# Kernel optimization log

Measured on AMD Instinct MI355X. Metric: run time of the kernel, lower is better.

The kernel has to match this reference:

```python
import jax, jax.numpy as jnp
import numpy as np

N_NODES = 100000      # total nodes across batch (50 graphs x 2000 nodes)
N_EDGES = 1600000     # avg degree 16
D = 64                # input_dim = hidden dims = output_dim
L = 3                 # number of GIN layers actually executed
NUM_GRAPHS = 50
NODES_PER_GRAPH = 2000
CAT_D = L * D         # 192, concat of hidden layer outputs


def setup_inputs() -> dict:
    key = jax.random.key(0)
    ks = jax.random.split(key, 12)
    s = 1.0 / np.sqrt(D)          # torch Linear init scale
    s2 = 1.0 / np.sqrt(CAT_D)
    return {
        "x": jax.random.normal(ks[0], (N_NODES, D), jnp.float32),
        "edge_index": jax.random.randint(ks[1], (2, N_EDGES), 0, N_NODES),
        "edge_weight": jax.random.uniform(ks[2], (N_EDGES,), jnp.float32),
        "batch": jnp.repeat(jnp.arange(NUM_GRAPHS), NODES_PER_GRAPH),  # sorted graph ids
        "W1": jax.random.uniform(ks[3], (L, D, D), jnp.float32, -s, s),
        "b1": jax.random.uniform(ks[4], (L, D), jnp.float32, -s, s),
        "W2": jax.random.uniform(ks[5], (L, D, D), jnp.float32, -s, s),
        "b2": jax.random.uniform(ks[6], (L, D), jnp.float32, -s, s),
        "eps": jnp.zeros((L,), jnp.float32),  # train_eps init 0.0
        "lin_w": jax.random.uniform(ks[7], (CAT_D, D), jnp.float32, -s2, s2),
        "lin_b": jax.random.uniform(ks[8], (D,), jnp.float32, -s2, s2),
    }


def reference(x, edge_index, edge_weight, batch, W1, b1, W2, b2, eps, lin_w, lin_b):
    src, dst = edge_index[0], edge_index[1]
    ew = edge_weight[:, None]
    h = x
    hiddens = []
    for l in range(L):
        # weighted GIN: aggregate sum_j w_ij * h_j at destination nodes
        agg = jax.ops.segment_sum(h[src] * ew, dst, num_segments=N_NODES)
        z = (1.0 + eps[l]) * h + agg
        # GIN MLP: Linear -> LeakyReLU -> Linear
        z = jax.nn.leaky_relu(z @ W1[l] + b1[l]) @ W2[l] + b2[l]
        hiddens.append(z)              # hiddens store pre-activation conv output
        h = jax.nn.leaky_relu(z)       # activation feeds next layer (dropout=0)
    h_cat = jnp.concatenate(hiddens, axis=-1)          # [N, 192]
    pooled = jax.ops.segment_sum(h_cat, batch, num_segments=NUM_GRAPHS)  # global_add_pool
    return pooled @ lin_w + lin_b                      # [NUM_GRAPHS, D]
```

## Files before the change

### kernel.cpp

```cpp
#include <hip/hip_runtime.h>

#define N_NODES 100000
#define N_EDGES 1600000
#define DD 64
#define NLAYER 3
#define NUM_GRAPHS 50
#define NODES_PER_GRAPH 2000
#define CAT_D (NLAYER * DD)
#define MROWS 80
#define MLP_THREADS 320
#define LPITCH 72

#define NPB 256
#define NB ((N_NODES + NPB - 1) / NPB)
#define BPAD 6144
#define ECHUNK 4096

#define GNODES 32
#define WECAP 288

typedef __attribute__((ext_vector_type(8))) short short8;
typedef __attribute__((ext_vector_type(4))) float float4v;

__device__ __forceinline__ unsigned short f2bf(float f) {
    unsigned u = __float_as_uint(f);
    unsigned r = u + 0x7FFF + ((u >> 16) & 1);
    return (unsigned short)(r >> 16);
}
__device__ __forceinline__ float bflo(unsigned u) {
    return __uint_as_float(u << 16);
}
__device__ __forceinline__ float bfhi(unsigned u) {
    return __uint_as_float(u & 0xFFFF0000u);
}

__global__ __launch_bounds__(256) void convert_x_kernel(
    const float* __restrict__ x, unsigned short* __restrict__ hx)
{
    int i = (blockIdx.x * blockDim.x + threadIdx.x) * 4;
    if (i + 3 < N_NODES * DD) {
        float4 v = *(const float4*)&x[i];
        hx[i]     = f2bf(v.x);
        hx[i + 1] = f2bf(v.y);
        hx[i + 2] = f2bf(v.z);
        hx[i + 3] = f2bf(v.w);
    }
}

__global__ __launch_bounds__(256) void convert_w_kernel(
    const float* __restrict__ W1, const float* __restrict__ W2,
    unsigned short* __restrict__ W1t, unsigned short* __restrict__ W2t,
    int* __restrict__ cursor)
{
    int idx = blockIdx.x * blockDim.x + threadIdx.x;
    if (idx < NB) cursor[idx] = idx * BPAD;
    if (idx >= 2 * NLAYER * DD * DD) return;
    int which = idx / (NLAYER * DD * DD);
    int rem = idx % (NLAYER * DD * DD);
    int l = rem / (DD * DD);
    int t = rem % (DD * DD);
    int n = t >> 6, k = t & 63;
    const float* W = which ? W2 : W1;
    unsigned short* Wt = which ? W2t : W1t;
    Wt[l * DD * DD + n * DD + k] = f2bf(W[l * DD * DD + k * DD + n]);
}

__global__ __launch_bounds__(256) void bin_kernel(
    const int* __restrict__ src, const int* __restrict__ dst,
    const float* __restrict__ ew, int* __restrict__ cursor,
    uint2* __restrict__ binned)
{
    __shared__ uint2 stage[ECHUNK];
    __shared__ unsigned short bkt[ECHUNK];
    __shared__ int cnt[512];
    __shared__ int base[512];
    __shared__ int ssum[256];
    __shared__ int gbase[512];

    const int tid = threadIdx.x;
    const int start = blockIdx.x * ECHUNK;
    const int count = min(ECHUNK, N_EDGES - start);

    cnt[tid] = 0;
    cnt[tid + 256] = 0;
    __syncthreads();

    unsigned pk1[16], pk2[16];
    int eb[16], er[16];
    #pragma unroll
    for (int k = 0; k < 16; ++k) {
        int i = tid + k * 256;
        if (i < count) {
            int e = start + i;
            int s = src[e];
            int d = dst[e];
            float w = ew[e];
            int b = d >> 8;
            pk1[k] = (unsigned)s | ((unsigned)(d & 255) << 17);
            pk2[k] = __float_as_uint(w);
            eb[k] = b;
            er[k] = atomicAdd(&cnt[b], 1);
        } else {
            eb[k] = -1;
        }
    }
    __syncthreads();

    int c0 = cnt[2 * tid], c1 = cnt[2 * tid + 1];
    ssum[tid] = c0 + c1;
    __syncthreads();
    for (int off = 1; off < 256; off <<= 1) {
        int x = (tid >= off) ? ssum[tid - off] : 0;
        __syncthreads();
        ssum[tid] += x;
        __syncthreads();
    }
    int ex = (tid > 0) ? ssum[tid - 1] : 0;
    base[2 * tid] = ex;
    base[2 * tid + 1] = ex + c0;

    if (2 * tid < NB && c0 > 0)     gbase[2 * tid]     = atomicAdd(&cursor[2 * tid], c0);
    if (2 * tid + 1 < NB && c1 > 0) gbase[2 * tid + 1] = atomicAdd(&cursor[2 * tid + 1], c1);
    __syncthreads();

    #pragma unroll
    for (int k = 0; k < 16; ++k) {
        if (eb[k] >= 0) {
            int p = base[eb[k]] + er[k];
            stage[p].x = pk1[k];
            stage[p].y = pk2[k];
            bkt[p] = (unsigned short)eb[k];
        }
    }
    __syncthreads();

    for (int i = tid; i < count; i += 256) {
        int b = bkt[i];
        binned[gbase[b] + (i - base[b])] = stage[i];
    }
}

__global__ __launch_bounds__(256) void localsort_kernel(
    const int* __restrict__ cursor, const uint2* __restrict__ binned,
    uint2* __restrict__ s_edge, int* __restrict__ beg, int* __restrict__ end)
{
    __shared__ int deg[NPB];
    __shared__ int rb[NPB];
    __shared__ int cur[NPB];

    const int nb = blockIdx.x;
    const int tid = threadIdx.x;
    const int bstart = nb * BPAD;
    const int count = cursor[nb] - bstart;

    deg[tid] = 0;
    __syncthreads();
    for (int i = tid; i < count; i += 256) {
        unsigned w = binned[bstart + i].x;
        atomicAdd(&deg[(w >> 17) & 255], 1);
    }
    __syncthreads();

    int v = deg[tid];
    rb[tid] = v;
    __syncthreads();
    for (int off = 1; off < 256; off <<= 1) {
        int x = (tid >= off) ? rb[tid - off] : 0;
        __syncthreads();
        rb[tid] += x;
        __syncthreads();
    }
    int ex = rb[tid] - v;
    cur[tid] = ex;
    int node = nb * NPB + tid;
    if (node < N_NODES) {
        beg[node] = bstart + ex;
        end[node] = bstart + ex + v;
    }
    __syncthreads();

    for (int i = tid; i < count; i += 256) {
        uint2 e = binned[bstart + i];
        int d = (e.x >> 17) & 255;
        int r = atomicAdd(&cur[d], 1);
        uint2 o;
        o.x = e.x & 0x1FFFF;
        o.y = e.y;
        s_edge[bstart + r] = o;
    }
}

__global__ __launch_bounds__(256) void gather_kernel(
    const uint4* __restrict__ h4, const int* __restrict__ beg,
    const int* __restrict__ end, const uint2* __restrict__ s_edge,
    const float* __restrict__ eps, int l, uint4* __restrict__ z4)
{
    __shared__ uint2 eds[4 * WECAP];

    const int w    = threadIdx.x >> 6;
    const int lane = threadIdx.x & 63;
    const int o    = lane >> 3;
    const int fl   = lane & 7;
    const int nbase = blockIdx.x * GNODES + w * 8;
    const int node  = nbase + o;

    const int ebeg = beg[nbase];
    const int cnt  = end[nbase + 7] - ebeg;
    uint2* wl = &eds[w * WECAP];
    const bool lds_ok = (cnt <= WECAP);
    if (lds_ok) {
        for (int i = lane; i < cnt; i += 64) wl[i] = s_edge[ebeg + i];
    }

    const int gbeg = beg[node];
    const int deg  = end[node] - gbeg;

    float acc[4][8];
    #pragma unroll
    for (int c = 0; c < 4; ++c)
        #pragma unroll
        for (int j = 0; j < 8; ++j) acc[c][j] = 0.f;

    const uint4* hfl = h4 + fl;

    if (lds_ok) {
        const int bi = gbeg - ebeg;
        for (int it = 0; it < deg; it += 4) {
            #pragma unroll
            for (int c = 0; c < 4; ++c) {
                bool ok = (it + c) < deg;
                int idx = ok ? (bi + it + c) : bi;
                uint2 p = wl[idx];
                float wv = ok ? __uint_as_float(p.y) : 0.f;
                uint4 r = hfl[(long)p.x * 8];
                acc[c][0] += bflo(r.x) * wv;  acc[c][1] += bfhi(r.x) * wv;
                acc[c][2] += bflo(r.y) * wv;  acc[c][3] += bfhi(r.y) * wv;
                acc[c][4] += bflo(r.z) * wv;  acc[c][5] += bfhi(r.z) * wv;
                acc[c][6] += bflo(r.w) * wv;  acc[c][7] += bfhi(r.w) * wv;
            }
        }
    } else {
        for (int it = 0; it < deg; it += 4) {
            #pragma unroll
            for (int c = 0; c < 4; ++c) {
                bool ok = (it + c) < deg;
                int idx = ok ? (gbeg + it + c) : gbeg;
                uint2 p = s_edge[idx];
                float wv = ok ? __uint_as_float(p.y) : 0.f;
                uint4 r = hfl[(long)p.x * 8];
                acc[c][0] += bflo(r.x) * wv;  acc[c][1] += bfhi(r.x) * wv;
                acc[c][2] += bflo(r.y) * wv;  acc[c][3] += bfhi(r.y) * wv;
                acc[c][4] += bflo(r.z) * wv;  acc[c][5] += bfhi(r.z) * wv;
                acc[c][6] += bflo(r.w) * wv;  acc[c][7] += bfhi(r.w) * wv;
            }
        }
    }

    float s[8];
    #pragma unroll
    for (int j = 0; j < 8; ++j)
        s[j] = (acc[0][j] + acc[1][j]) + (acc[2][j] + acc[3][j]);

    const float e1 = 1.0f + eps[l];
    uint4 selfr = hfl[(long)node * 8];
    float z0 = e1 * bflo(selfr.x) + s[0];
    float z1 = e1 * bfhi(selfr.x) + s[1];
    float z2 = e1 * bflo(selfr.y) + s[2];
    float z3 = e1 * bfhi(selfr.y) + s[3];
    float z4v = e1 * bflo(selfr.z) + s[4];
    float z5 = e1 * bfhi(selfr.z) + s[5];
    float z6 = e1 * bflo(selfr.w) + s[6];
    float z7 = e1 * bfhi(selfr.w) + s[7];
    uint4 ov;
    ov.x = (unsigned)f2bf(z0) | ((unsigned)f2bf(z1) << 16);
    ov.y = (unsigned)f2bf(z2) | ((unsigned)f2bf(z3) << 16);
    ov.z = (unsigned)f2bf(z4v) | ((unsigned)f2bf(z5) << 16);
    ov.w = (unsigned)f2bf(z6) | ((unsigned)f2bf(z7) << 16);
    z4[(long)node * 8 + fl] = ov;
}

__global__ __launch_bounds__(MLP_THREADS) void mlp_kernel(
    const unsigned short* __restrict__ z_in,
    const unsigned short* __restrict__ W1t, const unsigned short* __restrict__ W2t,
    const float* __restrict__ b1l, const float* __restrict__ b2l,
    int l, unsigned short* __restrict__ h_out, float* __restrict__ pooled)
{
    __shared__ __align__(16) unsigned short zs[MROWS * LPITCH];
    __shared__ __align__(16) unsigned short w1s[DD * LPITCH];
    __shared__ __align__(16) unsigned short w2s[DD * LPITCH];
    __shared__ float red[5 * DD];

    const int tid  = threadIdx.x;
    const int lane = tid & 63;
    const int w    = tid >> 6;
    const int m15  = lane & 15;
    const int quad = lane >> 4;
    const long base = (long)blockIdx.x * MROWS;

    for (int idx = tid; idx < MROWS * 8; idx += MLP_THREADS) {
        int row = idx >> 3, seg = idx & 7;
        *(int4*)&zs[row * LPITCH + seg * 8] =
            *(const int4*)&z_in[(base + row) * DD + seg * 8];
    }
    for (int idx = tid; idx < DD * 8; idx += MLP_THREADS) {
        int row = idx >> 3, seg = idx & 7;
        *(int4*)&w1s[row * LPITCH + seg * 8] =
            *(const int4*)&W1t[(size_t)l * DD * DD + row * DD + seg * 8];
        *(int4*)&w2s[row * LPITCH + seg * 8] =
            *(const int4*)&W2t[(size_t)l * DD * DD + row * DD + seg * 8];
    }
    __syncthreads();

    {
        short8 a0 = *(const short8*)&zs[(w * 16 + m15) * LPITCH + quad * 8];
        short8 a1 = *(const short8*)&zs[(w * 16 + m15) * LPITCH + 32 + quad * 8];
        #pragma unroll
        for (int n = 0; n < 4; ++n) {
            short8 b0 = *(const short8*)&w1s[(n * 16 + m15) * LPITCH + quad * 8];
            short8 b1 = *(const short8*)&w1s[(n * 16 + m15) * LPITCH + 32 + quad * 8];
            float4v acc = {0.f, 0.f, 0.f, 0.f};
            acc = __builtin_amdgcn_mfma_f32_16x16x32_bf16(a0, b0, acc, 0, 0, 0);
            acc = __builtin_amdgcn_mfma_f32_16x16x32_bf16(a1, b1, acc, 0, 0, 0);
            int col = n * 16 + m15;
            float bv = b1l[col];
            #pragma unroll
            for (int r = 0; r < 4; ++r) {
                int row = w * 16 + quad * 4 + r;
                float t = acc[r] + bv;
                t = t > 0.0f ? t : 0.01f * t;
                zs[row * LPITCH + col] = f2bf(t);
            }
        }
    }

    float psum[4];
    {
        short8 a0 = *(const short8*)&zs[(w * 16 + m15) * LPITCH + quad * 8];
        short8 a1 = *(const short8*)&zs[(w * 16 + m15) * LPITCH + 32 + quad * 8];
        #pragma unroll
        for (int n = 0; n < 4; ++n) {
            short8 b0 = *(const short8*)&w2s[(n * 16 + m15) * LPITCH + quad * 8];
            short8 b1 = *(const short8*)&w2s[(n * 16 + m15) * LPITCH + 32 + quad * 8];
            float4v acc = {0.f, 0.f, 0.f, 0.f};
            acc = __builtin_amdgcn_mfma_f32_16x16x32_bf16(a0, b0, acc, 0, 0, 0);
            acc = __builtin_amdgcn_mfma_f32_16x16x32_bf16(a1, b1, acc, 0, 0, 0);
            int col = n * 16 + m15;
            float bv = b2l[col];
            float ps = 0.0f;
            #pragma unroll
            for (int r = 0; r < 4; ++r) {
                int row = w * 16 + quad * 4 + r;
                float z2 = acc[r] + bv;
                ps += z2;
                float hv = z2 > 0.0f ? z2 : 0.01f * z2;
                zs[row * LPITCH + col] = f2bf(hv);
            }
            psum[n] = ps;
        }
    }
    #pragma unroll
    for (int n = 0; n < 4; ++n) {
        float v = psum[n];
        v += __shfl_xor(v, 16);
        v += __shfl_xor(v, 32);
        if (quad == 0) red[w * DD + n * 16 + m15] = v;
    }
    __syncthreads();

    if (h_out) {
        for (int idx = tid; idx < MROWS * 8; idx += MLP_THREADS) {
            int row = idx >> 3, seg = idx & 7;
            *(int4*)&h_out[(base + row) * DD + seg * 8] =
                *(const int4*)&zs[row * LPITCH + seg * 8];
        }
    }
    if (tid < DD) {
        float tot = red[tid] + red[DD + tid] + red[2 * DD + tid]
                  + red[3 * DD + tid] + red[4 * DD + tid];
        int g = blockIdx.x / (NODES_PER_GRAPH / MROWS);
        atomicAdd(&pooled[g * CAT_D + l * DD + tid], tot);
    }
}

__global__ __launch_bounds__(64) void final_kernel(
    const float* __restrict__ pooled, const float* __restrict__ lin_w,
    const float* __restrict__ lin_b, float* __restrict__ out)
{
    int g = blockIdx.x;
    int j = threadIdx.x;
    float acc = lin_b[j];
    for (int k = 0; k < CAT_D; ++k)
        acc += pooled[g * CAT_D + k] * lin_w[k * DD + j];
    out[g * DD + j] = acc;
}

extern "C" void kernel_launch(void* const* d_in, const int* in_sizes, int n_in,
                              void* d_out, int out_size, void* d_ws, size_t ws_size,
                              hipStream_t stream)
{
    const float* x     = (const float*)d_in[0];
    const int*   ei    = (const int*)d_in[1];
    const float* ew    = (const float*)d_in[2];
    const float* W1    = (const float*)d_in[4];
    const float* b1    = (const float*)d_in[5];
    const float* W2    = (const float*)d_in[6];
    const float* b2    = (const float*)d_in[7];
    const float* eps   = (const float*)d_in[8];
    const float* lin_w = (const float*)d_in[9];
    const float* lin_b = (const float*)d_in[10];
    float* out = (float*)d_out;

    const int* src = ei;
    const int* dst = ei + N_EDGES;

    char* wsb = (char*)d_ws;
    size_t off = 0;
    auto alloc = [&](size_t bytes) -> void* {
        off = (off + 15) & ~(size_t)15;
        void* p = wsb + off;
        off += bytes;
        return p;
    };
    unsigned short* hX   = (unsigned short*)alloc((size_t)N_NODES * DD * 2);
    unsigned short* hA   = (unsigned short*)alloc((size_t)N_NODES * DD * 2);
    unsigned short* zbuf = (unsigned short*)alloc((size_t)N_NODES * DD * 2);
    unsigned short* W1t  = (unsigned short*)alloc((size_t)NLAYER * DD * DD * 2);
    unsigned short* W2t  = (unsigned short*)alloc((size_t)NLAYER * DD * DD * 2);
    float* pooled        = (float*)alloc((size_t)NUM_GRAPHS * CAT_D * 4);
    int*   cursor        = (int*)alloc((size_t)NB * 4);
    int*   beg           = (int*)alloc((size_t)N_NODES * 4);
    int*   end_          = (int*)alloc((size_t)N_NODES * 4);
    uint2* binned        = (uint2*)alloc((size_t)NB * BPAD * 8);
    uint2* s_edge        = (uint2*)alloc((size_t)NB * BPAD * 8);

    convert_x_kernel<<<(N_NODES * DD / 4 + 255) / 256, 256, 0, stream>>>(x, hX);
    convert_w_kernel<<<(2 * NLAYER * DD * DD + 255) / 256, 256, 0, stream>>>(
        W1, W2, W1t, W2t, cursor);

    bin_kernel<<<(N_EDGES + ECHUNK - 1) / ECHUNK, 256, 0, stream>>>(
        src, dst, ew, cursor, binned);
    localsort_kernel<<<NB, 256, 0, stream>>>(cursor, binned, s_edge, beg, end_);

    hipMemsetAsync(pooled, 0, NUM_GRAPHS * CAT_D * sizeof(float), stream);

    const unsigned short* h_ins[3]  = { hX, hA, hX };
    unsigned short*       h_outs[3] = { hA, hX, nullptr };
    for (int l = 0; l < NLAYER; ++l) {
        gather_kernel<<<N_NODES / GNODES, 256, 0, stream>>>(
            (const uint4*)h_ins[l], beg, end_, s_edge, eps, l,
            (uint4*)zbuf);

        mlp_kernel<<<N_NODES / MROWS, MLP_THREADS, 0, stream>>>(
            zbuf, W1t, W2t,
            b1 + (size_t)l * DD, b2 + (size_t)l * DD,
            l, h_outs[l], pooled);
    }

    final_kernel<<<NUM_GRAPHS, 64, 0, stream>>>(pooled, lin_w, lin_b, out);
}
```

Measured before the change: 277.3 us.

## Store node features in fp8 and pack edge index with bf16 weight

Node feature buffers are now stored as fp8 (e4m3 via the cvt_pk_fp8 builtins) instead of bf16, which halves the bytes fetched per neighbour in the gather. The sorted edge records shrink from 8 to 4 bytes by packing a 17-bit source index with a 15-bit truncated bf16 weight. The per-warp LDS edge cache capacity is enlarged to match. These changes target the memory-bound gather, but fp8 features and a sign-dropped, truncated weight lose considerable precision and may break the accuracy tolerance.

```diff
diff --git a/kernel.cpp b/kernel.cpp
--- a/kernel.cpp
+++ b/kernel.cpp
@@ -17,10 +17,11 @@
 #define ECHUNK 4096
 
 #define GNODES 32
-#define WECAP 288
+#define WECAP 384
 
 typedef __attribute__((ext_vector_type(8))) short short8;
 typedef __attribute__((ext_vector_type(4))) float float4v;
+typedef __attribute__((ext_vector_type(2))) float float2v;
 
 __device__ __forceinline__ unsigned short f2bf(float f) {
     unsigned u = __float_as_uint(f);
@@ -35,15 +36,19 @@
 }
 
 __global__ __launch_bounds__(256) void convert_x_kernel(
-    const float* __restrict__ x, unsigned short* __restrict__ hx)
-{
-    int i = (blockIdx.x * blockDim.x + threadIdx.x) * 4;
-    if (i + 3 < N_NODES * DD) {
-        float4 v = *(const float4*)&x[i];
-        hx[i]     = f2bf(v.x);
-        hx[i + 1] = f2bf(v.y);
-        hx[i + 2] = f2bf(v.z);
-        hx[i + 3] = f2bf(v.w);
+    const float* __restrict__ x, uint2* __restrict__ hx8)
+{
+    int i = blockIdx.x * blockDim.x + threadIdx.x;
+    if (i < N_NODES * DD / 8) {
+        const float4* xp = (const float4*)(x + (size_t)i * 8);
+        float4 a = xp[0], b = xp[1];
+        int lo = 0, hi = 0;
+        lo = __builtin_amdgcn_cvt_pk_fp8_f32(a.x, a.y, lo, 0);
+        lo = __builtin_amdgcn_cvt_pk_fp8_f32(a.z, a.w, lo, 1);
+        hi = __builtin_amdgcn_cvt_pk_fp8_f32(b.x, b.y, hi, 0);
+        hi = __builtin_amdgcn_cvt_pk_fp8_f32(b.z, b.w, hi, 1);
+        uint2 o; o.x = (unsigned)lo; o.y = (unsigned)hi;
+        hx8[i] = o;
     }
 }
 
@@ -142,7 +147,7 @@
 
 __global__ __launch_bounds__(256) void localsort_kernel(
     const int* __restrict__ cursor, const uint2* __restrict__ binned,
-    uint2* __restrict__ s_edge, int* __restrict__ beg, int* __restrict__ end)
+    unsigned* __restrict__ s_edge, int* __restrict__ beg, int* __restrict__ end)
 {
     __shared__ int deg[NPB];
     __shared__ int rb[NPB];
@@ -183,19 +188,17 @@
         uint2 e = binned[bstart + i];
         int d = (e.x >> 17) & 255;
         int r = atomicAdd(&cur[d], 1);
-        uint2 o;
-        o.x = e.x & 0x1FFFF;
-        o.y = e.y;
-        s_edge[bstart + r] = o;
+        unsigned wb = (unsigned)f2bf(__uint_as_float(e.y)) & 0x7FFF;
+        s_edge[bstart + r] = (e.x & 0x1FFFF) | (wb << 17);
     }
 }
 
 __global__ __launch_bounds__(256) void gather_kernel(
-    const uint4* __restrict__ h4, const int* __restrict__ beg,
-    const int* __restrict__ end, const uint2* __restrict__ s_edge,
+    const uint2* __restrict__ h8, const int* __restrict__ beg,
+    const int* __restrict__ end, const unsigned* __restrict__ s_edge,
     const float* __restrict__ eps, int l, uint4* __restrict__ z4)
 {
-    __shared__ uint2 eds[4 * WECAP];
+    __shared__ unsigned eds[4 * WECAP];
 
     const int w    = threadIdx.x >> 6;
     const int lane = threadIdx.x & 63;
@@ -206,7 +209,7 @@
 
     const int ebeg = beg[nbase];
     const int cnt  = end[nbase + 7] - ebeg;
-    uint2* wl = &eds[w * WECAP];
+    unsigned* wl = &eds[w * WECAP];
     const bool lds_ok = (cnt <= WECAP);
     if (lds_ok) {
         for (int i = lane; i < cnt; i += 64) wl[i] = s_edge[ebeg + i];
@@ -221,7 +224,7 @@
         #pragma unroll
         for (int j = 0; j < 8; ++j) acc[c][j] = 0.f;
 
-    const uint4* hfl = h4 + fl;
+    const uint2* hfl = h8 + fl;
 
     if (lds_ok) {
         const int bi = gbeg - ebeg;
@@ -230,13 +233,17 @@
             for (int c = 0; c < 4; ++c) {
                 bool ok = (it + c) < deg;
                 int idx = ok ? (bi + it + c) : bi;
-                uint2 p = wl[idx];
-                float wv = ok ? __uint_as_float(p.y) : 0.f;
-                uint4 r = hfl[(long)p.x * 8];
-                acc[c][0] += bflo(r.x) * wv;  acc[c][1] += bfhi(r.x) * wv;
-                acc[c][2] += bflo(r.y) * wv;  acc[c][3] += bfhi(r.y) * wv;
-                acc[c][4] += bflo(r.z) * wv;  acc[c][5] += bfhi(r.z) * wv;
-                acc[c][6] += bflo(r.w) * wv;  acc[c][7] += bfhi(r.w) * wv;
+                unsigned p = wl[idx];
+                float wv = ok ? __uint_as_float((p >> 17) << 16) : 0.f;
+                uint2 r = hfl[(long)(p & 0x1FFFF) * 8];
+                float2v f01 = __builtin_amdgcn_cvt_pk_f32_fp8(r.x, false);
+                float2v f23 = __builtin_amdgcn_cvt_pk_f32_fp8(r.x, true);
+                float2v f45 = __builtin_amdgcn_cvt_pk_f32_fp8(r.y, false);
+                float2v f67 = __builtin_amdgcn_cvt_pk_f32_fp8(r.y, true);
+                acc[c][0] += f01.x * wv;  acc[c][1] += f01.y * wv;
+                acc[c][2] += f23.x * wv;  acc[c][3] += f23.y * wv;
+                acc[c][4] += f45.x * wv;  acc[c][5] += f45.y * wv;
+                acc[c][6] += f67.x * wv;  acc[c][7] += f67.y * wv;
             }
         }
     } else {
@@ -245,13 +252,17 @@
             for (int c = 0; c < 4; ++c) {
                 bool ok = (it + c) < deg;
                 int idx = ok ? (gbeg + it + c) : gbeg;
-                uint2 p = s_edge[idx];
-                float wv = ok ? __uint_as_float(p.y) : 0.f;
-                uint4 r = hfl[(long)p.x * 8];
-                acc[c][0] += bflo(r.x) * wv;  acc[c][1] += bfhi(r.x) * wv;
-                acc[c][2] += bflo(r.y) * wv;  acc[c][3] += bfhi(r.y) * wv;
-                acc[c][4] += bflo(r.z) * wv;  acc[c][5] += bfhi(r.z) * wv;
-                acc[c][6] += bflo(r.w) * wv;  acc[c][7] += bfhi(r.w) * wv;
+                unsigned p = s_edge[idx];
+                float wv = ok ? __uint_as_float((p >> 17) << 16) : 0.f;
+                uint2 r = hfl[(long)(p & 0x1FFFF) * 8];
+                float2v f01 = __builtin_amdgcn_cvt_pk_f32_fp8(r.x, false);
+                float2v f23 = __builtin_amdgcn_cvt_pk_f32_fp8(r.x, true);
+                float2v f45 = __builtin_amdgcn_cvt_pk_f32_fp8(r.y, false);
+                float2v f67 = __builtin_amdgcn_cvt_pk_f32_fp8(r.y, true);
+                acc[c][0] += f01.x * wv;  acc[c][1] += f01.y * wv;
+                acc[c][2] += f23.x * wv;  acc[c][3] += f23.y * wv;
+                acc[c][4] += f45.x * wv;  acc[c][5] += f45.y * wv;
+                acc[c][6] += f67.x * wv;  acc[c][7] += f67.y * wv;
             }
         }
     }
@@ -262,15 +273,19 @@
         s[j] = (acc[0][j] + acc[1][j]) + (acc[2][j] + acc[3][j]);
 
     const float e1 = 1.0f + eps[l];
-    uint4 selfr = hfl[(long)node * 8];
-    float z0 = e1 * bflo(selfr.x) + s[0];
-    float z1 = e1 * bfhi(selfr.x) + s[1];
-    float z2 = e1 * bflo(selfr.y) + s[2];
-    float z3 = e1 * bfhi(selfr.y) + s[3];
-    float z4v = e1 * bflo(selfr.z) + s[4];
-    float z5 = e1 * bfhi(selfr.z) + s[5];
-    float z6 = e1 * bflo(selfr.w) + s[6];
-    float z7 = e1 * bfhi(selfr.w) + s[7];
+    uint2 selfr = hfl[(long)node * 8];
+    float2v s01 = __builtin_amdgcn_cvt_pk_f32_fp8(selfr.x, false);
+    float2v s23 = __builtin_amdgcn_cvt_pk_f32_fp8(selfr.x, true);
+    float2v s45 = __builtin_amdgcn_cvt_pk_f32_fp8(selfr.y, false);
+    float2v s67 = __builtin_amdgcn_cvt_pk_f32_fp8(selfr.y, true);
+    float z0 = e1 * s01.x + s[0];
+    float z1 = e1 * s01.y + s[1];
+    float z2 = e1 * s23.x + s[2];
+    float z3 = e1 * s23.y + s[3];
+    float z4v = e1 * s45.x + s[4];
+    float z5 = e1 * s45.y + s[5];
+    float z6 = e1 * s67.x + s[6];
+    float z7 = e1 * s67.y + s[7];
     uint4 ov;
     ov.x = (unsigned)f2bf(z0) | ((unsigned)f2bf(z1) << 16);
     ov.y = (unsigned)f2bf(z2) | ((unsigned)f2bf(z3) << 16);
@@ -283,7 +298,7 @@
     const unsigned short* __restrict__ z_in,
     const unsigned short* __restrict__ W1t, const unsigned short* __restrict__ W2t,
     const float* __restrict__ b1l, const float* __restrict__ b2l,
-    int l, unsigned short* __restrict__ h_out, float* __restrict__ pooled)
+    int l, uint2* __restrict__ h_out8, float* __restrict__ pooled)
 {
     __shared__ __align__(16) unsigned short zs[MROWS * LPITCH];
     __shared__ __align__(16) unsigned short w1s[DD * LPITCH];
@@ -367,11 +382,17 @@
     }
     __syncthreads();
 
-    if (h_out) {
+    if (h_out8) {
         for (int idx = tid; idx < MROWS * 8; idx += MLP_THREADS) {
             int row = idx >> 3, seg = idx & 7;
-            *(int4*)&h_out[(base + row) * DD + seg * 8] =
-                *(const int4*)&zs[row * LPITCH + seg * 8];
+            int4 v = *(const int4*)&zs[row * LPITCH + seg * 8];
+            int lo = 0, hi = 0;
+            lo = __builtin_amdgcn_cvt_pk_fp8_f32(bflo((unsigned)v.x), bfhi((unsigned)v.x), lo, 0);
+            lo = __builtin_amdgcn_cvt_pk_fp8_f32(bflo((unsigned)v.y), bfhi((unsigned)v.y), lo, 1);
+            hi = __builtin_amdgcn_cvt_pk_fp8_f32(bflo((unsigned)v.z), bfhi((unsigned)v.z), hi, 0);
+            hi = __builtin_amdgcn_cvt_pk_fp8_f32(bflo((unsigned)v.w), bfhi((unsigned)v.w), hi, 1);
+            uint2 o; o.x = (unsigned)lo; o.y = (unsigned)hi;
+            h_out8[(base + row) * 8 + seg] = o;
         }
     }
     if (tid < DD) {
@@ -421,8 +442,8 @@
         off += bytes;
         return p;
     };
-    unsigned short* hX   = (unsigned short*)alloc((size_t)N_NODES * DD * 2);
-    unsigned short* hA   = (unsigned short*)alloc((size_t)N_NODES * DD * 2);
+    uint2*  hX    = (uint2*)alloc((size_t)N_NODES * DD);
+    uint2*  hA    = (uint2*)alloc((size_t)N_NODES * DD);
     unsigned short* zbuf = (unsigned short*)alloc((size_t)N_NODES * DD * 2);
     unsigned short* W1t  = (unsigned short*)alloc((size_t)NLAYER * DD * DD * 2);
     unsigned short* W2t  = (unsigned short*)alloc((size_t)NLAYER * DD * DD * 2);
@@ -431,9 +452,9 @@
     int*   beg           = (int*)alloc((size_t)N_NODES * 4);
     int*   end_          = (int*)alloc((size_t)N_NODES * 4);
     uint2* binned        = (uint2*)alloc((size_t)NB * BPAD * 8);
-    uint2* s_edge        = (uint2*)alloc((size_t)NB * BPAD * 8);
-
-    convert_x_kernel<<<(N_NODES * DD / 4 + 255) / 256, 256, 0, stream>>>(x, hX);
+    unsigned* s_edge     = (unsigned*)alloc((size_t)NB * BPAD * 4);
+
+    convert_x_kernel<<<(N_NODES * DD / 8 + 255) / 256, 256, 0, stream>>>(x, hX);
     convert_w_kernel<<<(2 * NLAYER * DD * DD + 255) / 256, 256, 0, stream>>>(
         W1, W2, W1t, W2t, cursor);
 
@@ -443,12 +464,11 @@
 
     hipMemsetAsync(pooled, 0, NUM_GRAPHS * CAT_D * sizeof(float), stream);
 
-    const unsigned short* h_ins[3]  = { hX, hA, hX };
-    unsigned short*       h_outs[3] = { hA, hX, nullptr };
+    const uint2* h_ins[3]  = { hX, hA, hX };
+    uint2*       h_outs[3] = { hA, hX, nullptr };
     for (int l = 0; l < NLAYER; ++l) {
         gather_kernel<<<N_NODES / GNODES, 256, 0, stream>>>(
-            (const uint4*)h_ins[l], beg, end_, s_edge, eps, l,
-            (uint4*)zbuf);
+            h_ins[l], beg, end_, s_edge, eps, l, (uint4*)zbuf);
 
         mlp_kernel<<<N_NODES / MROWS, MLP_THREADS, 0, stream>>>(
             zbuf, W1t, W2t,
```

Result: faster. 244.8 us (-11.7%).
